# Kernel optimization log

Measured on AMD Instinct MI355X. Metric: run time of the kernel, lower is better.

## Reference

```python
import jax, jax.numpy as jnp
import numpy as np

NUM_HEADS = 8
NUM_LEVELS = 4
NUM_POINTS = 8
SPATIAL_SHAPES = np.array([[92, 160], [46, 80], [23, 40], [12, 20]], dtype=np.int64)


def _bilinear_sample(val_hw, loc, Hl, Wl):
    """val_hw: (bs, heads, H*W, d); loc: (bs, nq, heads, P, 2) in [0,1].
    Matches torch grid_sample(bilinear, zeros padding, align_corners=False)
    applied to grid = 2*loc - 1, i.e. pixel coords x = loc_x*W - 0.5.
    Returns (bs, heads, nq, P, d)."""
    x = loc[..., 0] * Wl - 0.5
    y = loc[..., 1] * Hl - 0.5
    x0 = jnp.floor(x)
    y0 = jnp.floor(y)
    wx = (x - x0).transpose(0, 2, 1, 3)  # (bs, heads, nq, P)
    wy = (y - y0).transpose(0, 2, 1, 3)
    x0i = x0.astype(jnp.int32).transpose(0, 2, 1, 3)
    y0i = y0.astype(jnp.int32).transpose(0, 2, 1, 3)

    def gather(ix, iy):
        valid = ((ix >= 0) & (ix < Wl) & (iy >= 0) & (iy < Hl)).astype(val_hw.dtype)
        idx = jnp.clip(iy, 0, Hl - 1) * Wl + jnp.clip(ix, 0, Wl - 1)  # (bs,heads,nq,P)
        b, h, nq, P = idx.shape
        g = jnp.take_along_axis(val_hw, idx.reshape(b, h, nq * P, 1), axis=2)
        return g.reshape(b, h, nq, P, -1) * valid[..., None]

    return (gather(x0i, y0i) * ((1 - wx) * (1 - wy))[..., None]
            + gather(x0i + 1, y0i) * (wx * (1 - wy))[..., None]
            + gather(x0i, y0i + 1) * ((1 - wx) * wy)[..., None]
            + gather(x0i + 1, y0i + 1) * (wx * wy)[..., None])


def setup_inputs() -> dict:
    key = jax.random.key(0)
    ks = jax.random.split(key, 10)
    C = 256
    bs, nq = 2, 10000
    nv = int((SPATIAL_SHAPES[:, 0] * SPATIAL_SHAPES[:, 1]).sum())  # 19560
    s = 1.0 / np.sqrt(C)
    return {
        "query": jax.random.normal(ks[0], (bs, nq, C), dtype=jnp.float32),
        "value": jax.random.normal(ks[1], (bs, nv, C), dtype=jnp.float32),
        "reference_points": jax.random.uniform(ks[2], (bs, nq, 4, 2), dtype=jnp.float32),
        "spatial_shapes": SPATIAL_SHAPES,
        "W_value": jax.random.normal(ks[3], (C, C), dtype=jnp.float32) * s,
        "b_value": jnp.zeros((C,), dtype=jnp.float32),
        "W_off": jax.random.normal(ks[4], (C, NUM_HEADS * NUM_LEVELS * NUM_POINTS * 2), dtype=jnp.float32) * 0.01,
        "b_off": jax.random.normal(ks[5], (NUM_HEADS * NUM_LEVELS * NUM_POINTS * 2,), dtype=jnp.float32) * 0.1,
        "W_attn": jax.random.normal(ks[6], (C, NUM_HEADS * NUM_LEVELS * NUM_POINTS), dtype=jnp.float32) * s,
        "b_attn": jnp.zeros((NUM_HEADS * NUM_LEVELS * NUM_POINTS,), dtype=jnp.float32),
    }


def reference(query, value, reference_points, spatial_shapes,
              W_value, b_value, W_off, b_off, W_attn, b_attn):
    bs, nq, C = query.shape
    NH, NL, NP = NUM_HEADS, NUM_LEVELS, NUM_POINTS
    d = C // NH
    Z = reference_points.shape[2]  # num_Z_anchors
    shapes_np = np.asarray(spatial_shapes)  # static host-side shapes

    # value / offset / attention projections
    v = (value @ W_value + b_value).reshape(bs, -1, NH, d)
    off = (query @ W_off + b_off).reshape(bs, nq, NH, NL, NP, 2)
    attn = jax.nn.softmax((query @ W_attn + b_attn).reshape(bs, nq, NH, NL * NP), axis=-1)
    attn = attn.reshape(bs, nq, NH, NL, NP)

    # normalize offsets by (W, H) per level and add to reference points
    norm = jnp.stack([spatial_shapes[:, 1], spatial_shapes[:, 0]], -1).astype(query.dtype)  # (NL, 2)
    off = off / norm[None, None, None, :, None, :]
    off = off.reshape(bs, nq, NH, NL, NP // Z, Z, 2)
    loc = reference_points[:, :, None, None, None, :, :] + off  # (bs,nq,NH,NL,NP//Z,Z,2)
    loc = loc.reshape(bs, nq, NH, NL, NP, 2)

    out = jnp.zeros((bs, NH, nq, d), dtype=query.dtype)
    start = 0
    for l in range(NL):
        Hl, Wl = int(shapes_np[l, 0]), int(shapes_np[l, 1])
        v_l = v[:, start:start + Hl * Wl].transpose(0, 2, 1, 3)  # (bs, NH, H*W, d)
        start += Hl * Wl
        sampled = _bilinear_sample(v_l, loc[:, :, :, l], Hl, Wl)  # (bs,NH,nq,NP,d)
        out = out + jnp.einsum('bhqpd,bqhp->bhqd', sampled, attn[:, :, :, l])
    return out.transpose(0, 2, 1, 3).reshape(bs, nq, NH * d)
```

## Files before the change

### kernel.cpp

```cpp
#include <hip/hip_runtime.h>
#include <math.h>

#define NH 8
#define NL 4
#define NP 8
#define CDIM 256
#define NQ 10000
#define BS 2
#define NV 19560

__constant__ int LVL_H[NL]     = {92, 46, 23, 12};
__constant__ int LVL_W[NL]     = {160, 80, 40, 20};
__constant__ int LVL_START[NL] = {0, 14720, 18400, 19320};

typedef __attribute__((ext_vector_type(8))) short short8;
typedef __attribute__((ext_vector_type(4))) float f32x4;

__device__ __forceinline__ unsigned short f2bf(float f) {
    unsigned int u = __float_as_uint(f);
    u += 0x7fffu + ((u >> 16) & 1u);
    return (unsigned short)(u >> 16);
}

__global__ __launch_bounds__(256) void concat_wb(
    const float* __restrict__ W_off, const float* __restrict__ b_off,
    const float* __restrict__ W_attn, const float* __restrict__ b_attn,
    float* __restrict__ Bcat, float* __restrict__ bias_cat)
{
    const int k = blockIdx.x;
    const int t = threadIdx.x;
    #pragma unroll
    for (int s = 0; s < 3; s++) {
        const int n = s * 256 + t;
        float v;
        if (k < 256)
            v = (n < 512) ? W_off[k * 512 + n] : W_attn[k * 256 + (n - 512)];
        else
            v = (n < 512) ? b_off[n] : b_attn[n - 512];
        if (k < 256) Bcat[k * 768 + n] = v;
        else         bias_cat[n] = v;
    }
}

#define AST 130
template <int MODE>
__global__ __launch_bounds__(256) void gemm_bias_mfma(
    const float* __restrict__ A, const float* __restrict__ B,
    const float* __restrict__ bias, float* __restrict__ Cf,
    unsigned short* __restrict__ Cbf, int M, int N)
{
    __shared__ short8 Al[4 * AST];
    __shared__ short8 Bl[4 * AST];

    const int t = threadIdx.x;
    const int rowBase = blockIdx.x * 128;
    const int colBase = blockIdx.y * 128;

    const int w  = t >> 6;
    const int l  = t & 63;
    const int wm = (w >> 1) * 64;
    const int wn = (w & 1) * 64;
    const int row16 = l & 15;
    const int kg    = l >> 4;

    const int ar  = t >> 2;
    const int akg = t & 3;
    const int bn   = t & 127;
    const int bkg0 = (t >> 7) * 2;

    f32x4 acc[4][4] = {};

    for (int k0 = 0; k0 < 256; k0 += 32) {
        #pragma unroll
        for (int pass = 0; pass < 2; pass++) {
            const int r = pass * 64 + ar;
            const int grow = rowBase + r;
            float va[8];
            if (grow < M) {
                const float* ap = A + (size_t)grow * 256 + k0 + akg * 8;
                float4 f0 = *(const float4*)ap;
                float4 f1 = *(const float4*)(ap + 4);
                va[0]=f0.x; va[1]=f0.y; va[2]=f0.z; va[3]=f0.w;
                va[4]=f1.x; va[5]=f1.y; va[6]=f1.z; va[7]=f1.w;
            } else {
                #pragma unroll
                for (int e = 0; e < 8; e++) va[e] = 0.f;
            }
            short8 v;
            #pragma unroll
            for (int e = 0; e < 8; e++) v[e] = (short)f2bf(va[e]);
            Al[akg * AST + r] = v;
        }
        #pragma unroll
        for (int it = 0; it < 2; it++) {
            const int kgc = bkg0 + it;
            const float* bp = B + (size_t)(k0 + kgc * 8) * N + colBase + bn;
            short8 v;
            #pragma unroll
            for (int e = 0; e < 8; e++) v[e] = (short)f2bf(bp[(size_t)e * N]);
            Bl[kgc * AST + bn] = v;
        }
        __syncthreads();

        short8 af[4], bfr[4];
        #pragma unroll
        for (int i = 0; i < 4; i++) af[i] = Al[kg * AST + wm + i * 16 + row16];
        #pragma unroll
        for (int j = 0; j < 4; j++) bfr[j] = Bl[kg * AST + wn + j * 16 + row16];
        #pragma unroll
        for (int i = 0; i < 4; i++)
            #pragma unroll
            for (int j = 0; j < 4; j++)
                acc[i][j] = __builtin_amdgcn_mfma_f32_16x16x32_bf16(
                    af[i], bfr[j], acc[i][j], 0, 0, 0);
        __syncthreads();
    }

    const int crow0 = rowBase + wm + (l >> 4) * 4;
    const int ccol0 = colBase + wn + (l & 15);
    float bv[4];
    #pragma unroll
    for (int j = 0; j < 4; j++) bv[j] = bias[ccol0 + j * 16];
    #pragma unroll
    for (int i = 0; i < 4; i++) {
        #pragma unroll
        for (int r = 0; r < 4; r++) {
            const int row = crow0 + i * 16 + r;
            if (row >= M) continue;
            #pragma unroll
            for (int j = 0; j < 4; j++) {
                const float val = acc[i][j][r] + bv[j];
                const int col = ccol0 + j * 16;
                if (MODE == 0) {
                    Cf[(size_t)row * N + col] = val;
                } else {
                    const int b   = row / NV;
                    const int pix = row - b * NV;
                    const int h   = col >> 5;
                    const int ch  = col & 31;
                    Cbf[((size_t)(b * NH + h) * NV + pix) * 32 + ch] = f2bf(val);
                }
            }
        }
    }
}

__global__ __launch_bounds__(256) void sample_kernel(
    const unsigned short* __restrict__ vproj,
    const float* __restrict__ offcat,
    const float* __restrict__ refpts,
    float* __restrict__ out)
{
    const int bid = blockIdx.x;
    const int h   = bid & 7;
    const int g   = bid >> 3;
    const int b   = g & 1;
    const int q0  = (g >> 1) * 8;
    const int t   = threadIdx.x;

    __shared__ float4 desc[8 * 64];

    const int qi = t >> 5, j = t & 31;
    const int qrow = b * NQ + q0 + qi;

    {
        const int lv = j >> 3, p = j & 7;

        float logit = offcat[(size_t)qrow * 768 + 512 + h * 32 + j];
        float m = logit;
        #pragma unroll
        for (int s = 16; s > 0; s >>= 1) m = fmaxf(m, __shfl_xor(m, s, 32));
        float e = __expf(logit - m);
        float ssum = e;
        #pragma unroll
        for (int s = 16; s > 0; s >>= 1) ssum += __shfl_xor(ssum, s, 32);
        const float aw = e / ssum;

        const int Wl = LVL_W[lv], Hl = LVL_H[lv], st = LVL_START[lv];
        const float offx = offcat[(size_t)qrow * 768 + h * 64 + j * 2];
        const float offy = offcat[(size_t)qrow * 768 + h * 64 + j * 2 + 1];

        const int z = p & 3;
        const float rx = refpts[((size_t)qrow * 4 + z) * 2];
        const float ry = refpts[((size_t)qrow * 4 + z) * 2 + 1];

        const float x = fmaf(rx, (float)Wl, offx) - 0.5f;
        const float y = fmaf(ry, (float)Hl, offy) - 0.5f;
        const float x0f = floorf(x), y0f = floorf(y);
        const float wx = x - x0f, wy = y - y0f;
        const int x0 = (int)x0f, y0 = (int)y0f;

        const int xb = min(max(x0, 0), Wl - 2);
        const float wl = (x0 >= 0 && x0 < Wl)          ? (1.f - wx) : 0.f;
        const float wr = (x0 + 1 >= 0 && x0 + 1 < Wl)  ? wx         : 0.f;
        const float wA = (x0 == xb) ? wl : ((x0 + 1 == xb) ? wr : 0.f);
        const float wB = (x0 == xb) ? wr : ((x0 == xb + 1) ? wl : 0.f);

        #pragma unroll
        for (int r = 0; r < 2; r++) {
            const int yy = y0 + r;
            const float rwv = (yy >= 0 && yy < Hl)
                            ? (r ? wy : (1.f - wy)) * aw : 0.f;
            const int iy = min(max(yy, 0), Hl - 1);
            float4 d;
            d.x = __int_as_float(st + iy * Wl + xb);
            d.y = wA * rwv;
            d.z = wB * rwv;
            d.w = 0.f;
            desc[qi * 64 + j * 2 + r] = d;
        }
    }
    __syncthreads();

    const int lane = t & 31;
    const int grp  = lane >> 3;
    const int sub  = lane & 7;
    const int pix  = sub >> 2;
    const int chq  = sub & 3;

    const uint* slab = (const uint*)(vproj + (size_t)(b * NH + h) * NV * 32);
    const float4* dq = &desc[qi * 64];

    float acc[8] = {};
    #pragma unroll 4
    for (int i = 0; i < 16; i++) {
        const float4 dsc = dq[i * 4 + grp];
        const int   lidx = __float_as_int(dsc.x);
        const float w    = pix ? dsc.z : dsc.y;
        const uint4 v = *(const uint4*)(slab + (size_t)(lidx + pix) * 16 + chq * 4);
        acc[0] += w * __uint_as_float(v.x << 16);
        acc[1] += w * __uint_as_float(v.x & 0xffff0000u);
        acc[2] += w * __uint_as_float(v.y << 16);
        acc[3] += w * __uint_as_float(v.y & 0xffff0000u);
        acc[4] += w * __uint_as_float(v.z << 16);
        acc[5] += w * __uint_as_float(v.z & 0xffff0000u);
        acc[6] += w * __uint_as_float(v.w << 16);
        acc[7] += w * __uint_as_float(v.w & 0xffff0000u);
    }

    #pragma unroll
    for (int s = 4; s <= 16; s <<= 1)
        #pragma unroll
        for (int e = 0; e < 8; e++) acc[e] += __shfl_xor(acc[e], s, 32);

    if ((lane & 0x1C) == 0) {
        float* op = out + (size_t)qrow * 256 + h * 32 + chq * 8;
        *(float4*)op       = make_float4(acc[0], acc[1], acc[2], acc[3]);
        *(float4*)(op + 4) = make_float4(acc[4], acc[5], acc[6], acc[7]);
    }
}

extern "C" void kernel_launch(void* const* d_in, const int* in_sizes, int n_in,
                              void* d_out, int out_size, void* d_ws, size_t ws_size,
                              hipStream_t stream)
{
    const float* query   = (const float*)d_in[0];
    const float* value   = (const float*)d_in[1];
    const float* refpts  = (const float*)d_in[2];
    const float* W_value = (const float*)d_in[4];
    const float* b_value = (const float*)d_in[5];
    const float* W_off   = (const float*)d_in[6];
    const float* b_off   = (const float*)d_in[7];
    const float* W_attn  = (const float*)d_in[8];
    const float* b_attn  = (const float*)d_in[9];

    unsigned short* vproj = (unsigned short*)d_ws;
    float* offcat  = (float*)((char*)d_ws + 20029440);
    float* Bcat    = (float*)((char*)d_ws + 20029440 + 61440000);
    float* biascat = Bcat + 256 * 768;

    const dim3 blk(256);

    concat_wb<<<dim3(257), blk, 0, stream>>>(W_off, b_off, W_attn, b_attn,
                                             Bcat, biascat);

    gemm_bias_mfma<1><<<dim3((BS * NV + 127) / 128, 2), blk, 0, stream>>>(
        value, W_value, b_value, nullptr, vproj, BS * NV, CDIM);

    gemm_bias_mfma<0><<<dim3((BS * NQ + 127) / 128, 6), blk, 0, stream>>>(
        query, Bcat, biascat, offcat, nullptr, BS * NQ, 768);

    sample_kernel<<<dim3(BS * NQ), blk, 0, stream>>>(
        vproj, offcat, refpts, (float*)d_out);
}
```

Measured before the change: 227.8 us.

## Pre-convert inputs and weights to bf16, store GEMM outputs as fp16

Value and query are converted to bf16 in standalone kernels, and the weights are pre-transposed to bf16, so the GEMMs load short8 vectors directly and skip per-tile conversion and strided B loads. GEMM outputs (projected values and offsets/logits) are now written as fp16 instead of fp32/bf16, which halves the offcat traffic read by the sampler. In exchange, it adds extra conversion passes over value and query that write and reread their data, and fp16 offsets could lose precision for large offset values.

```diff
diff --git a/kernel.cpp b/kernel.cpp
--- a/kernel.cpp
+++ b/kernel.cpp
@@ -15,6 +15,7 @@
 
 typedef __attribute__((ext_vector_type(8))) short short8;
 typedef __attribute__((ext_vector_type(4))) float f32x4;
+typedef __attribute__((ext_vector_type(8))) _Float16 half8;
 
 __device__ __forceinline__ unsigned short f2bf(float f) {
     unsigned int u = __float_as_uint(f);
@@ -22,32 +23,46 @@
     return (unsigned short)(u >> 16);
 }
 
-__global__ __launch_bounds__(256) void concat_wb(
-    const float* __restrict__ W_off, const float* __restrict__ b_off,
-    const float* __restrict__ W_attn, const float* __restrict__ b_attn,
-    float* __restrict__ Bcat, float* __restrict__ bias_cat)
-{
-    const int k = blockIdx.x;
+__global__ __launch_bounds__(256) void cvt_bf16(
+    const float* __restrict__ src, unsigned short* __restrict__ dst, int n4)
+{
+    const int i = blockIdx.x * 256 + threadIdx.x;
+    if (i >= n4) return;
+    const float4 f = ((const float4*)src)[i];
+    ushort4 o;
+    o.x = f2bf(f.x); o.y = f2bf(f.y); o.z = f2bf(f.z); o.w = f2bf(f.w);
+    ((ushort4*)dst)[i] = o;
+}
+
+__global__ __launch_bounds__(256) void prep_weights(
+    const float* __restrict__ Wv,
+    const float* __restrict__ Woff, const float* __restrict__ boff,
+    const float* __restrict__ Wattn, const float* __restrict__ battn,
+    unsigned short* __restrict__ BvalT, unsigned short* __restrict__ BcatT,
+    float* __restrict__ biascat)
+{
+    const int n = blockIdx.x;
     const int t = threadIdx.x;
-    #pragma unroll
-    for (int s = 0; s < 3; s++) {
-        const int n = s * 256 + t;
-        float v;
-        if (k < 256)
-            v = (n < 512) ? W_off[k * 512 + n] : W_attn[k * 256 + (n - 512)];
-        else
-            v = (n < 512) ? b_off[n] : b_attn[n - 512];
-        if (k < 256) Bcat[k * 768 + n] = v;
-        else         bias_cat[n] = v;
+    if (n < 256) {
+        BvalT[n * 256 + t] = f2bf(Wv[t * 256 + n]);
+    } else if (n < 1024) {
+        const int m = n - 256;
+        const float v = (m < 512) ? Woff[t * 512 + m] : Wattn[t * 256 + (m - 512)];
+        BcatT[m * 256 + t] = f2bf(v);
+    } else {
+        #pragma unroll
+        for (int s = 0; s < 3; s++) {
+            const int i = s * 256 + t;
+            biascat[i] = (i < 512) ? boff[i] : battn[i - 512];
+        }
     }
 }
 
 #define AST 130
 template <int MODE>
 __global__ __launch_bounds__(256) void gemm_bias_mfma(
-    const float* __restrict__ A, const float* __restrict__ B,
-    const float* __restrict__ bias, float* __restrict__ Cf,
-    unsigned short* __restrict__ Cbf, int M, int N)
+    const unsigned short* __restrict__ A, const unsigned short* __restrict__ Bt,
+    const float* __restrict__ bias, _Float16* __restrict__ Ch, int M, int N)
 {
     __shared__ short8 Al[4 * AST];
     __shared__ short8 Bl[4 * AST];
@@ -63,42 +78,27 @@
     const int row16 = l & 15;
     const int kg    = l >> 4;
 
-    const int ar  = t >> 2;
-    const int akg = t & 3;
-    const int bn   = t & 127;
-    const int bkg0 = (t >> 7) * 2;
+    const int sr = t >> 1;
+    const int sh = t & 1;
 
     f32x4 acc[4][4] = {};
 
     for (int k0 = 0; k0 < 256; k0 += 32) {
-        #pragma unroll
-        for (int pass = 0; pass < 2; pass++) {
-            const int r = pass * 64 + ar;
-            const int grow = rowBase + r;
-            float va[8];
+        {
+            const int grow = rowBase + sr;
+            short8 v0 = {}, v1 = {};
             if (grow < M) {
-                const float* ap = A + (size_t)grow * 256 + k0 + akg * 8;
-                float4 f0 = *(const float4*)ap;
-                float4 f1 = *(const float4*)(ap + 4);
-                va[0]=f0.x; va[1]=f0.y; va[2]=f0.z; va[3]=f0.w;
-                va[4]=f1.x; va[5]=f1.y; va[6]=f1.z; va[7]=f1.w;
-            } else {
-                #pragma unroll
-                for (int e = 0; e < 8; e++) va[e] = 0.f;
+                const unsigned short* ap = A + (size_t)grow * 256 + k0 + sh * 16;
+                v0 = *(const short8*)ap;
+                v1 = *(const short8*)(ap + 8);
             }
-            short8 v;
-            #pragma unroll
-            for (int e = 0; e < 8; e++) v[e] = (short)f2bf(va[e]);
-            Al[akg * AST + r] = v;
-        }
-        #pragma unroll
-        for (int it = 0; it < 2; it++) {
-            const int kgc = bkg0 + it;
-            const float* bp = B + (size_t)(k0 + kgc * 8) * N + colBase + bn;
-            short8 v;
-            #pragma unroll
-            for (int e = 0; e < 8; e++) v[e] = (short)f2bf(bp[(size_t)e * N]);
-            Bl[kgc * AST + bn] = v;
+            Al[(sh * 2 + 0) * AST + sr] = v0;
+            Al[(sh * 2 + 1) * AST + sr] = v1;
+        }
+        {
+            const unsigned short* bp = Bt + (size_t)(colBase + sr) * 256 + k0 + sh * 16;
+            Bl[(sh * 2 + 0) * AST + sr] = *(const short8*)bp;
+            Bl[(sh * 2 + 1) * AST + sr] = *(const short8*)(bp + 8);
         }
         __syncthreads();
 
@@ -132,13 +132,13 @@
                 const float val = acc[i][j][r] + bv[j];
                 const int col = ccol0 + j * 16;
                 if (MODE == 0) {
-                    Cf[(size_t)row * N + col] = val;
+                    Ch[(size_t)row * N + col] = (_Float16)val;
                 } else {
                     const int b   = row / NV;
                     const int pix = row - b * NV;
                     const int h   = col >> 5;
                     const int ch  = col & 31;
-                    Cbf[((size_t)(b * NH + h) * NV + pix) * 32 + ch] = f2bf(val);
+                    Ch[((size_t)(b * NH + h) * NV + pix) * 32 + ch] = (_Float16)val;
                 }
             }
         }
@@ -146,8 +146,8 @@
 }
 
 __global__ __launch_bounds__(256) void sample_kernel(
-    const unsigned short* __restrict__ vproj,
-    const float* __restrict__ offcat,
+    const _Float16* __restrict__ vproj,
+    const _Float16* __restrict__ offcat,
     const float* __restrict__ refpts,
     float* __restrict__ out)
 {
@@ -166,7 +166,7 @@
     {
         const int lv = j >> 3, p = j & 7;
 
-        float logit = offcat[(size_t)qrow * 768 + 512 + h * 32 + j];
+        float logit = (float)offcat[(size_t)qrow * 768 + 512 + h * 32 + j];
         float m = logit;
         #pragma unroll
         for (int s = 16; s > 0; s >>= 1) m = fmaxf(m, __shfl_xor(m, s, 32));
@@ -177,8 +177,8 @@
         const float aw = e / ssum;
 
         const int Wl = LVL_W[lv], Hl = LVL_H[lv], st = LVL_START[lv];
-        const float offx = offcat[(size_t)qrow * 768 + h * 64 + j * 2];
-        const float offy = offcat[(size_t)qrow * 768 + h * 64 + j * 2 + 1];
+        const float offx = (float)offcat[(size_t)qrow * 768 + h * 64 + j * 2];
+        const float offy = (float)offcat[(size_t)qrow * 768 + h * 64 + j * 2 + 1];
 
         const int z = p & 3;
         const float rx = refpts[((size_t)qrow * 4 + z) * 2];
@@ -218,7 +218,7 @@
     const int pix  = sub >> 2;
     const int chq  = sub & 3;
 
-    const uint* slab = (const uint*)(vproj + (size_t)(b * NH + h) * NV * 32);
+    const _Float16* slab = vproj + (size_t)(b * NH + h) * NV * 32;
     const float4* dq = &desc[qi * 64];
 
     float acc[8] = {};
@@ -227,15 +227,10 @@
         const float4 dsc = dq[i * 4 + grp];
         const int   lidx = __float_as_int(dsc.x);
         const float w    = pix ? dsc.z : dsc.y;
-        const uint4 v = *(const uint4*)(slab + (size_t)(lidx + pix) * 16 + chq * 4);
-        acc[0] += w * __uint_as_float(v.x << 16);
-        acc[1] += w * __uint_as_float(v.x & 0xffff0000u);
-        acc[2] += w * __uint_as_float(v.y << 16);
-        acc[3] += w * __uint_as_float(v.y & 0xffff0000u);
-        acc[4] += w * __uint_as_float(v.z << 16);
-        acc[5] += w * __uint_as_float(v.z & 0xffff0000u);
-        acc[6] += w * __uint_as_float(v.w << 16);
-        acc[7] += w * __uint_as_float(v.w & 0xffff0000u);
+        const half8 v = *(const half8*)(slab + (size_t)(lidx + pix) * 32 + chq * 8);
+        #pragma unroll
+        for (int e = 0; e < 8; e++)
+            acc[e] += w * (float)v[e];
     }
 
     #pragma unroll
@@ -264,21 +259,28 @@
     const float* W_attn  = (const float*)d_in[8];
     const float* b_attn  = (const float*)d_in[9];
 
-    unsigned short* vproj = (unsigned short*)d_ws;
-    float* offcat  = (float*)((char*)d_ws + 20029440);
-    float* Bcat    = (float*)((char*)d_ws + 20029440 + 61440000);
-    float* biascat = Bcat + 256 * 768;
+    char* ws = (char*)d_ws;
+    _Float16*       vproj   = (_Float16*)(ws);
+    unsigned short* valuebf = (unsigned short*)(ws + 20029440);
+    unsigned short* querybf = (unsigned short*)(ws + 40058880);
+    _Float16*       offcat  = (_Float16*)(ws + 50298880);
+    unsigned short* BvalT   = (unsigned short*)(ws + 81018880);
+    unsigned short* BcatT   = (unsigned short*)(ws + 81149952);
+    float*          biascat = (float*)(ws + 81543168);
 
     const dim3 blk(256);
 
-    concat_wb<<<dim3(257), blk, 0, stream>>>(W_off, b_off, W_attn, b_attn,
-                                             Bcat, biascat);
+    cvt_bf16<<<dim3(9780), blk, 0, stream>>>(value, valuebf, BS * NV * 256 / 4);
+    cvt_bf16<<<dim3(5000), blk, 0, stream>>>(query, querybf, BS * NQ * 256 / 4);
+    prep_weights<<<dim3(1025), blk, 0, stream>>>(W_value, W_off, b_off,
+                                                 W_attn, b_attn,
+                                                 BvalT, BcatT, biascat);
 
     gemm_bias_mfma<1><<<dim3((BS * NV + 127) / 128, 2), blk, 0, stream>>>(
-        value, W_value, b_value, nullptr, vproj, BS * NV, CDIM);
+        valuebf, BvalT, b_value, vproj, BS * NV, CDIM);
 
     gemm_bias_mfma<0><<<dim3((BS * NQ + 127) / 128, 6), blk, 0, stream>>>(
-        query, Bcat, biascat, offcat, nullptr, BS * NQ, 768);
+        querybf, BcatT, biascat, offcat, BS * NQ, 768);
 
     sample_kernel<<<dim3(BS * NQ), blk, 0, stream>>>(
         vproj, offcat, refpts, (float*)d_out);
```

After: 225.0 us. No clear change (-1.2%).
